# Optimization experiments

Measured on AMD Instinct MI355X. Metric: run time of the kernel, lower is better.

## Reference

```python
import jax, jax.numpy as jnp
import numpy as np

N = 50000      # nodes
E = 800000     # edges (before self-loops)
IN = 256       # in_channels
H = 4          # heads (layer 1)
C = 64         # hidden per head
OUT = 40       # out_channels / classes


def setup_inputs() -> dict:
    key = jax.random.key(0)
    ks = jax.random.split(key, 10)
    s = 0.05  # weight init scale
    return {
        "x": jax.random.normal(ks[0], (N, IN), jnp.float32),
        "edge_index": jax.random.randint(ks[1], (2, E), 0, N),
        "W1": jax.random.normal(ks[2], (IN, H * C), jnp.float32) * s,
        "a_src1": jax.random.normal(ks[3], (H, C), jnp.float32) * s,
        "a_dst1": jax.random.normal(ks[4], (H, C), jnp.float32) * s,
        "b1": jnp.zeros((H * C,), jnp.float32),
        "W2": jax.random.normal(ks[5], (H * C, OUT), jnp.float32) * s,
        "a_src2": jax.random.normal(ks[6], (1, OUT), jnp.float32) * s,
        "a_dst2": jax.random.normal(ks[7], (1, OUT), jnp.float32) * s,
        "b2": jnp.zeros((OUT,), jnp.float32),
    }


def _gat_layer(x, src, dst, W, a_src, a_dst, bias, heads, out_c):
    """PyG GATConv (concat=True, negative_slope=0.2, self-loops already in src/dst)."""
    n = x.shape[0]
    h = (x @ W).reshape(n, heads, out_c)                    # [N,H,C]
    al_s = jnp.sum(h * a_src, axis=-1)                      # [N,H]
    al_d = jnp.sum(h * a_dst, axis=-1)                      # [N,H]
    e = jax.nn.leaky_relu(al_s[src] + al_d[dst], 0.2)       # [Etot,H]
    # edge softmax over incoming edges of each destination node
    m = jax.ops.segment_max(e, dst, num_segments=n)         # [N,H]
    ee = jnp.exp(e - m[dst])
    denom = jax.ops.segment_sum(ee, dst, num_segments=n)
    alpha = ee / (denom[dst] + 1e-16)                       # [Etot,H]
    msg = alpha[:, :, None] * h[src]                        # [Etot,H,C]
    out = jax.ops.segment_sum(msg, dst, num_segments=n)     # [N,H,C]
    return out.reshape(n, heads * out_c) + bias


def reference(x, edge_index, W1, a_src1, a_dst1, b1, W2, a_src2, a_dst2, b2):
    n = x.shape[0]
    loops = jnp.arange(n, dtype=edge_index.dtype)
    src = jnp.concatenate([edge_index[0], loops])
    dst = jnp.concatenate([edge_index[1], loops])
    h = _gat_layer(x, src, dst, W1, a_src1, a_dst1, b1, H, C)   # [N, H*C]
    h = jax.nn.relu(h)
    # F.dropout in eval mode is identity (reference run in eval mode)
    out = _gat_layer(h, src, dst, W2, a_src2, a_dst2, b2, 1, OUT)  # [N, OUT]
    return jax.nn.log_softmax(out, axis=1)
```

## Files before the change

kernel.cpp:

```cpp
#include <hip/hip_runtime.h>
#include <hip/hip_bf16.h>

typedef __hip_bfloat16 bf16;
typedef short v8s __attribute__((ext_vector_type(8)));
typedef float v4f __attribute__((ext_vector_type(4)));

constexpr int NN    = 50000;
constexpr int NE    = 800000;
constexpr int CIN   = 256;
constexpr int HC    = 256;
constexpr int NH    = 4;
constexpr int NOUT  = 40;
constexpr int NPAD  = 48;
constexpr int SCB   = 196;
constexpr int B1    = 128;
constexpr int CH    = (NE + B1 - 1) / B1;
constexpr int NB    = (NN + 255) >> 8;

constexpr size_t al256(size_t x){ return (x + 255) & ~(size_t)255; }
constexpr size_t WS_FLAGS = 0;
constexpr size_t WS_EW1   = 256;
constexpr size_t WS_W1T   = al256(WS_EW1   + (size_t)NE*16);
constexpr size_t WS_AS1N  = al256(WS_W1T   + (size_t)CIN*HC*2);
constexpr size_t WS_AD1N  = al256(WS_AS1N  + HC*2);
constexpr size_t WS_B1N   = al256(WS_AD1N  + HC*2);
constexpr size_t WS_W2T   = al256(WS_B1N   + HC*2);
constexpr size_t WS_AS2N  = al256(WS_W2T   + (size_t)NPAD*HC*2);
constexpr size_t WS_AD2N  = al256(WS_AS2N  + NOUT*2);
constexpr size_t WS_B2N   = al256(WS_AD2N  + NOUT*2);
constexpr size_t WS_COUNTS= al256(WS_B2N   + NOUT*2);
constexpr size_t WS_CURSOR= al256(WS_COUNTS+ (size_t)NN*4);
constexpr size_t WS_ROWPTR= al256(WS_CURSOR+ (size_t)NN*4);
constexpr size_t WS_EIDX  = al256(WS_ROWPTR+ (size_t)(NN+1)*4);
constexpr size_t WS_H1    = al256(WS_EIDX  + (size_t)NE*4);
constexpr size_t WS_ALS1  = al256(WS_H1    + (size_t)NN*HC);
constexpr size_t WS_ALD1  = al256(WS_ALS1  + (size_t)NN*NH*4);
constexpr size_t WS_Y1    = al256(WS_ALD1  + (size_t)NN*NH*4);
constexpr size_t WS_H2    = al256(WS_Y1    + (size_t)NN*HC*2);
constexpr size_t WS_ALS2  = al256(WS_H2    + (size_t)NN*64);
constexpr size_t WS_ALD2  = al256(WS_ALS2  + (size_t)NN*4);
constexpr size_t WS_EW2   = al256(WS_ALD2  + (size_t)NN*4);
constexpr size_t WS_BSUM  = al256(WS_EW2   + (size_t)NE*4);
constexpr size_t WS_BOFF  = al256(WS_BSUM  + 1024);
constexpr size_t WS_GCNT  = al256(WS_BOFF  + 1024);
constexpr size_t WS_ROFF  = al256(WS_GCNT  + (size_t)256*B1*4);
constexpr size_t WS_BBASE = al256(WS_ROFF  + (size_t)256*B1*4);
constexpr size_t WS_EBUF  = al256(WS_BBASE + 1056);

constexpr int CV_W1  = 0;
constexpr int CV_AS1 = CV_W1  + CIN*HC;
constexpr int CV_AD1 = CV_AS1 + HC;
constexpr int CV_B1  = CV_AD1 + HC;
constexpr int CV_W2  = CV_B1  + HC;
constexpr int CV_AS2 = CV_W2  + HC*NOUT;
constexpr int CV_AD2 = CV_AS2 + NOUT;
constexpr int CV_B2  = CV_AD2 + NOUT;
constexpr int CV_HIST= CV_B2  + NOUT;
constexpr int CV_END = CV_HIST + NE;

__device__ __forceinline__ float b2f(bf16 v) { return __bfloat162float(v); }
__device__ __forceinline__ bf16  f2b(float v){ return __float2bfloat16(v); }
__device__ __forceinline__ float bits2f(unsigned short u){ return __uint_as_float(((unsigned)u) << 16); }
__device__ __forceinline__ unsigned short f2bits(float v){
  bf16 t = __float2bfloat16(v);
  return *reinterpret_cast<unsigned short*>(&t);
}
__device__ __forceinline__ float lrelu(float x){ return x > 0.f ? x : 0.2f * x; }

__device__ __forceinline__ float wave_sum(float v){
  #pragma unroll
  for (int off = 32; off; off >>= 1) v += __shfl_xor(v, off, 64);
  return v;
}
__device__ __forceinline__ float wave_max(float v){
  #pragma unroll
  for (int off = 32; off; off >>= 1) v = fmaxf(v, __shfl_xor(v, off, 64));
  return v;
}

__global__ __launch_bounds__(64) void k_detect(const unsigned short* __restrict__ xu,
                                               const unsigned* __restrict__ eu,
                                               int* __restrict__ flags){
  int lane = threadIdx.x;
  int cnt = 0;
  for (int i = lane; i < 256; i += 64){
    int e = (xu[i] >> 7) & 0xFF;
    cnt += (e >= 0x60 && e <= 0x8F) ? 1 : 0;
  }
  #pragma unroll
  for (int off = 32; off; off >>= 1) cnt += __shfl_xor(cnt, off, 64);
  unsigned odd = eu[2 * lane + 1];
  #pragma unroll
  for (int off = 32; off; off >>= 1) odd |= __shfl_xor(odd, off, 64);
  if (lane == 0){
    flags[0] = (cnt < 218) ? 1 : 0;
    flags[1] = (odd == 0)  ? 1 : 0;
  }
}

__device__ __forceinline__ bf16 cvt_b(const void* src, int i, int f32m){
  if (f32m) return __float2bfloat16(((const float*)src)[i]);
  return ((const bf16*)src)[i];
}

__global__ __launch_bounds__(256) void k_convert(
    const void* __restrict__ W1,
    const void* __restrict__ as1,const void* __restrict__ ad1,
    const void* __restrict__ b1, const void* __restrict__ W2,
    const void* __restrict__ as2,const void* __restrict__ ad2,
    const void* __restrict__ b2, const void* __restrict__ ei,
    char* __restrict__ ws){
  const int* flags = (const int*)(ws + WS_FLAGS);
  int f32m = flags[0], i64m = flags[1];
  bf16* w1t  = (bf16*)(ws + WS_W1T);
  bf16* as1n = (bf16*)(ws + WS_AS1N);
  bf16* ad1n = (bf16*)(ws + WS_AD1N);
  bf16* b1n  = (bf16*)(ws + WS_B1N);
  bf16* w2t  = (bf16*)(ws + WS_W2T);
  bf16* as2n = (bf16*)(ws + WS_AS2N);
  bf16* ad2n = (bf16*)(ws + WS_AD2N);
  bf16* b2n  = (bf16*)(ws + WS_B2N);
  int*  counts=(int*) (ws + WS_COUNTS);
  for (int g = blockIdx.x * 256 + threadIdx.x; g < CV_END; g += gridDim.x * 256){
    if      (g < CV_AS1){ int i = g-CV_W1; int k = i >> 8, n = i & 255;
      w1t[n*CIN + k] = cvt_b(W1, i, f32m); }
    else if (g < CV_AD1) as1n[g-CV_AS1] = cvt_b(as1,g-CV_AS1, f32m);
    else if (g < CV_B1 ) ad1n[g-CV_AD1] = cvt_b(ad1,g-CV_AD1, f32m);
    else if (g < CV_W2 ) b1n [g-CV_B1 ] = cvt_b(b1, g-CV_B1,  f32m);
    else if (g < CV_AS2){ int i = g-CV_W2; int k = i / NOUT, n = i - k*NOUT;
      w2t[n*CIN + k] = cvt_b(W2, i, f32m); }
    else if (g < CV_AD2) as2n[g-CV_AS2] = cvt_b(as2,g-CV_AS2, f32m);
    else if (g < CV_B2 ) ad2n[g-CV_AD2] = cvt_b(ad2,g-CV_AD2, f32m);
    else if (g < CV_HIST) b2n[g-CV_B2 ] = cvt_b(b2, g-CV_B2,  f32m);
    else { int i = g-CV_HIST;
      int d = i64m ? (int)((const long long*)ei)[(size_t)NE+i] : ((const int*)ei)[NE+i];
      atomicAdd(&counts[d], 1); }
  }
}

__global__ __launch_bounds__(256) void k_scan_part(const int* __restrict__ counts, int* __restrict__ bsum){
  __shared__ int lds[256];
  int t = threadIdx.x;
  int idx = blockIdx.x * 256 + t;
  int v = (idx < NN) ? counts[idx] : 0;
  lds[t] = v;
  #pragma unroll
  for (int s = 128; s > 0; s >>= 1){
    __syncthreads();
    if (t < s) lds[t] += lds[t + s];
  }
  if (t == 0) bsum[blockIdx.x] = lds[0];
}

__global__ __launch_bounds__(256) void k_scan_mid(const int* __restrict__ bsum, int* __restrict__ boff,
                                                  int* __restrict__ row_ptr){
  __shared__ int lds[256];
  int t = threadIdx.x;
  int v = (t < SCB) ? bsum[t] : 0;
  lds[t] = v;
  for (int off = 1; off < 256; off <<= 1){
    __syncthreads();
    int u = (t >= off) ? lds[t - off] : 0;
    __syncthreads();
    lds[t] += u;
  }
  __syncthreads();
  if (t < SCB) boff[t] = lds[t] - v;
  if (t == 0) row_ptr[NN] = NE;
}

__global__ __launch_bounds__(256) void k_scan_apply(const int* __restrict__ counts, const int* __restrict__ boff,
                                                    int* __restrict__ row_ptr){
  __shared__ int lds[256];
  int t = threadIdx.x;
  int idx = blockIdx.x * 256 + t;
  int v = (idx < NN) ? counts[idx] : 0;
  lds[t] = v;
  for (int off = 1; off < 256; off <<= 1){
    __syncthreads();
    int u = (t >= off) ? lds[t - off] : 0;
    __syncthreads();
    lds[t] += u;
  }
  __syncthreads();
  if (idx < NN) row_ptr[idx] = boff[blockIdx.x] + lds[t] - v;
}

__global__ __launch_bounds__(256) void k_lhist(const void* __restrict__ ei, const int* __restrict__ flags,
                                               int* __restrict__ gcnt){
  __shared__ int h[256];
  int tid = threadIdx.x, blk = blockIdx.x;
  h[tid] = 0;
  __syncthreads();
  int i0 = blk * CH, i1 = min(i0 + CH, NE);
  int i64m = flags[1];
  for (int i = i0 + tid; i < i1; i += 256){
    int d = i64m ? (int)((const long long*)ei)[(size_t)NE + i] : ((const int*)ei)[NE + i];
    atomicAdd(&h[d >> 8], 1);
  }
  __syncthreads();
  gcnt[tid * B1 + blk] = h[tid];
}

__global__ __launch_bounds__(256) void k_gscan(const int* __restrict__ gcnt, int* __restrict__ roff,
                                               int* __restrict__ bbase){
  __shared__ int lds[256];
  int t = threadIdx.x;
  int tot = 0;
  for (int blk = 0; blk < B1; ++blk) tot += gcnt[t * B1 + blk];
  lds[t] = tot;
  for (int off = 1; off < 256; off <<= 1){
    __syncthreads();
    int u = (t >= off) ? lds[t - off] : 0;
    __syncthreads();
    lds[t] += u;
  }
  __syncthreads();
  int base = lds[t] - tot;
  bbase[t] = base;
  if (t == 255) bbase[256] = NE;
  int run = base;
  for (int blk = 0; blk < B1; ++blk){
    roff[t * B1 + blk] = run;
    run += gcnt[t * B1 + blk];
  }
}

__global__ __launch_bounds__(256) void k_bscatter(const void* __restrict__ ei, const int* __restrict__ flags,
                                                  const int* __restrict__ roff, int2* __restrict__ ebuf){
  __shared__ int lcur[256];
  int tid = threadIdx.x, blk = blockIdx.x;
  lcur[tid] = roff[tid * B1 + blk];
  __syncthreads();
  int i0 = blk * CH, i1 = min(i0 + CH, NE);
  int i64m = flags[1];
  for (int i = i0 + tid; i < i1; i += 256){
    int s, d;
    if (i64m){ s = (int)((const long long*)ei)[i]; d = (int)((const long long*)ei)[(size_t)NE + i]; }
    else     { s = ((const int*)ei)[i];            d = ((const int*)ei)[NE + i]; }
    int pos = atomicAdd(&lcur[d >> 8], 1);
    ebuf[pos] = make_int2(s, d);
  }
}

__global__ __launch_bounds__(256) void k_refine(const int2* __restrict__ ebuf, const int* __restrict__ bbase,
                                                const int* __restrict__ row_ptr, int* __restrict__ cursor,
                                                int* __restrict__ eidx){
  int b = blockIdx.x;
  int p0 = bbase[b], p1 = bbase[b + 1];
  for (int p = p0 + threadIdx.x; p < p1; p += 256){
    int2 e = ebuf[p];
    int pos = row_ptr[e.y] + atomicAdd(&cursor[e.y], 1);
    eidx[pos] = e.x;
  }
}

constexpr int G1R = 64;
__global__ __launch_bounds__(256, 2) void k_gemm1(const void* __restrict__ xin,
                                               const int* __restrict__ flags,
                                               const bf16* __restrict__ w1t,
                                               const bf16* __restrict__ as1, const bf16* __restrict__ ad1,
                                               unsigned char* __restrict__ h1q,
                                               float* __restrict__ al_s1, float* __restrict__ al_d1){
  __shared__ __align__(16) short Ab[2][G1R * 64];
  __shared__ __align__(16) short Bb[2][256 * 64];
  int tid  = threadIdx.x;
  int w    = tid >> 6, lane = tid & 63, quad = lane >> 4, c = lane & 15;
  int row0 = blockIdx.x * G1R;
  int f32m = flags[0];

  v4f acc[4][4];
  #pragma unroll
  for (int mt = 0; mt < 4; ++mt)
    #pragma unroll
    for (int nt = 0; nt < 4; ++nt) acc[mt][nt] = (v4f){0.f,0.f,0.f,0.f};

  int arow = tid >> 2, aseg = tid & 3;
  int grow = row0 + arow; if (grow >= NN) grow = NN - 1;
  int asw  = arow & 7;
  int bsw  = tid & 7;

  float4 afl[4];
  v8s    abf[2];
  v8s    breg[8];

  auto loadA = [&](int ph){
    if (f32m){
      const float* src = (const float*)xin + (size_t)grow * CIN + ph*64 + aseg*16;
      #pragma unroll
      for (int i = 0; i < 4; ++i) afl[i] = *reinterpret_cast<const float4*>(src + i*4);
    } else {
      const short* src = (const short*)xin + (size_t)grow * CIN + ph*64 + aseg*16;
      abf[0] = *reinterpret_cast<const v8s*>(src);
      abf[1] = *reinterpret_cast<const v8s*>(src + 8);
    }
  };
  auto loadB = [&](int ph){
    const short* src = (const short*)w1t + (size_t)tid * CIN + ph*64;
    #pragma unroll
    for (int j = 0; j < 8; ++j) breg[j] = *reinterpret_cast<const v8s*>(src + j*8);
  };
  auto stageA = [&](int buf){
    short* dst = &Ab[buf][arow * 64];
    if (f32m){
      #pragma unroll
      for (int k = 0; k < 2; ++k){
        v8s t;
        t[0] = (short)f2bits(afl[2*k].x);   t[1] = (short)f2bits(afl[2*k].y);
        t[2] = (short)f2bits(afl[2*k].z);   t[3] = (short)f2bits(afl[2*k].w);
        t[4] = (short)f2bits(afl[2*k+1].x); t[5] = (short)f2bits(afl[2*k+1].y);
        t[6] = (short)f2bits(afl[2*k+1].z); t[7] = (short)f2bits(afl[2*k+1].w);
        *reinterpret_cast<v8s*>(dst + (((aseg*2 + k) ^ asw) << 3)) = t;
      }
    } else {
      #pragma unroll
      for (int k = 0; k < 2; ++k)
        *reinterpret_cast<v8s*>(dst + (((aseg*2 + k) ^ asw) << 3)) = abf[k];
    }
  };
  auto stageB = [&](int buf){
    short* dst = &Bb[buf][tid * 64];
    #pragma unroll
    for (int j = 0; j < 8; ++j)
      *reinterpret_cast<v8s*>(dst + ((j ^ bsw) << 3)) = breg[j];
  };

  loadA(0); loadB(0);
  stageA(0); stageB(0);
  __syncthreads();

  #pragma unroll
  for (int ph = 0; ph < 4; ++ph){
    int buf = ph & 1;
    if (ph < 3){ loadA(ph + 1); loadB(ph + 1); }
    #pragma unroll
    for (int s = 0; s < 2; ++s){
      int ch = s*4 + quad;
      int sl = (ch ^ (c & 7)) << 3;
      v8s af[4], bfb[4];
      #pragma unroll
      for (int mt = 0; mt < 4; ++mt)
        af[mt] = *reinterpret_cast<const v8s*>(&Ab[buf][(mt*16 + c) * 64 + sl]);
      #pragma unroll
      for (int nt = 0; nt < 4; ++nt)
        bfb[nt] = *reinterpret_cast<const v8s*>(&Bb[buf][(w*64 + nt*16 + c) * 64 + sl]);
      #pragma unroll
      for (int mt = 0; mt < 4; ++mt)
        #pragma unroll
        for (int nt = 0; nt < 4; ++nt)
          acc[mt][nt] = __builtin_amdgcn_mfma_f32_16x16x32_bf16(af[mt], bfb[nt], acc[mt][nt], 0, 0, 0);
    }
    if (ph < 3){
      stageA(buf ^ 1); stageB(buf ^ 1);
      __syncthreads();
    }
  }

  float as1v[4], ad1v[4];
  #pragma unroll
  for (int nt = 0; nt < 4; ++nt){
    as1v[nt] = b2f(as1[w*64 + nt*16 + c]);
    ad1v[nt] = b2f(ad1[w*64 + nt*16 + c]);
  }
  #pragma unroll
  for (int mt = 0; mt < 4; ++mt){
    #pragma unroll
    for (int r = 0; r < 4; ++r){
      float ps = 0.f, pd = 0.f;
      #pragma unroll
      for (int nt = 0; nt < 4; ++nt){ ps += acc[mt][nt][r] * as1v[nt]; pd += acc[mt][nt][r] * ad1v[nt]; }
      #pragma unroll
      for (int off = 1; off < 16; off <<= 1){ ps += __shfl_xor(ps, off, 64); pd += __shfl_xor(pd, off, 64); }
      int row = row0 + mt*16 + quad*4 + r;
      if (c == 0 && row < NN){
        al_s1[row * NH + w] = ps;
        al_d1[row * NH + w] = pd;
      }
    }
  }
  #pragma unroll
  for (int mt = 0; mt < 4; ++mt){
    #pragma unroll
    for (int nt = 0; nt < 4; ++nt){
      #pragma unroll
      for (int r = 0; r < 4; r += 2){
        int row = row0 + mt*16 + quad*4 + r;
        if (row + 1 < NN){
          int pk = __builtin_amdgcn_cvt_pk_fp8_f32(acc[mt][nt][r], acc[mt][nt][r+1], 0, false);
          size_t col = w*64 + nt*16 + c;
          h1q[(size_t)row       * HC + col] = (unsigned char)(pk & 0xFF);
          h1q[(size_t)(row + 1) * HC + col] = (unsigned char)((pk >> 8) & 0xFF);
        } else if (row < NN){
          int pk = __builtin_amdgcn_cvt_pk_fp8_f32(acc[mt][nt][r], acc[mt][nt][r], 0, false);
          h1q[(size_t)row * HC + w*64 + nt*16 + c] = (unsigned char)(pk & 0xFF);
        }
      }
    }
  }
}

__global__ __launch_bounds__(256) void k_gather1(const int* __restrict__ row_ptr, const int* __restrict__ eidx,
                                                 const float* __restrict__ al_s1, const float* __restrict__ al_d1,
                                                 const unsigned* __restrict__ h1v, const bf16* __restrict__ b1,
                                                 bf16* __restrict__ y1){
  int lane = threadIdx.x & 63;
  int n = blockIdx.x * 4 + (threadIdx.x >> 6);
  int h = lane >> 4;
  int p0 = __builtin_amdgcn_readfirstlane(row_ptr[n]);
  int p1 = __builtin_amdgcn_readfirstlane(row_ptr[n + 1]);
  float ad_h = al_d1[n * NH + h];
  float wss = __expf(lrelu(al_s1[n * NH + h] + ad_h));
  unsigned us = h1v[(size_t)n * 64 + lane];
  float den = wss;
  float a0 = wss * __builtin_amdgcn_cvt_f32_fp8(us, 0);
  float a1 = wss * __builtin_amdgcn_cvt_f32_fp8(us, 1);
  float a2 = wss * __builtin_amdgcn_cvt_f32_fp8(us, 2);
  float a3 = wss * __builtin_amdgcn_cvt_f32_fp8(us, 3);
  int p = p0;
  for (; p + 3 < p1; p += 4){
    int sA = __builtin_amdgcn_readfirstlane(eidx[p]);
    int sB = __builtin_amdgcn_readfirstlane(eidx[p + 1]);
    int sC = __builtin_amdgcn_readfirstlane(eidx[p + 2]);
    int sD = __builtin_amdgcn_readfirstlane(eidx[p + 3]);
    float wA = __expf(lrelu(al_s1[sA * NH + h] + ad_h));
    float wB = __expf(lrelu(al_s1[sB * NH + h] + ad_h));
    float wC = __expf(lrelu(al_s1[sC * NH + h] + ad_h));
    float wD = __expf(lrelu(al_s1[sD * NH + h] + ad_h));
    unsigned uA = h1v[(size_t)sA * 64 + lane];
    unsigned uB = h1v[(size_t)sB * 64 + lane];
    unsigned uC = h1v[(size_t)sC * 64 + lane];
    unsigned uD = h1v[(size_t)sD * 64 + lane];
    den += (wA + wB) + (wC + wD);
    a0 += wA * __builtin_amdgcn_cvt_f32_fp8(uA, 0) + wB * __builtin_amdgcn_cvt_f32_fp8(uB, 0)
        + wC * __builtin_amdgcn_cvt_f32_fp8(uC, 0) + wD * __builtin_amdgcn_cvt_f32_fp8(uD, 0);
    a1 += wA * __builtin_amdgcn_cvt_f32_fp8(uA, 1) + wB * __builtin_amdgcn_cvt_f32_fp8(uB, 1)
        + wC * __builtin_amdgcn_cvt_f32_fp8(uC, 1) + wD * __builtin_amdgcn_cvt_f32_fp8(uD, 1);
    a2 += wA * __builtin_amdgcn_cvt_f32_fp8(uA, 2) + wB * __builtin_amdgcn_cvt_f32_fp8(uB, 2)
        + wC * __builtin_amdgcn_cvt_f32_fp8(uC, 2) + wD * __builtin_amdgcn_cvt_f32_fp8(uD, 2);
    a3 += wA * __builtin_amdgcn_cvt_f32_fp8(uA, 3) + wB * __builtin_amdgcn_cvt_f32_fp8(uB, 3)
        + wC * __builtin_amdgcn_cvt_f32_fp8(uC, 3) + wD * __builtin_amdgcn_cvt_f32_fp8(uD, 3);
  }
  for (; p < p1; ++p){
    int s = __builtin_amdgcn_readfirstlane(eidx[p]);
    float w = __expf(lrelu(al_s1[s * NH + h] + ad_h));
    unsigned u = h1v[(size_t)s * 64 + lane];
    den += w;
    a0 += w * __builtin_amdgcn_cvt_f32_fp8(u, 0);
    a1 += w * __builtin_amdgcn_cvt_f32_fp8(u, 1);
    a2 += w * __builtin_amdgcn_cvt_f32_fp8(u, 2);
    a3 += w * __builtin_amdgcn_cvt_f32_fp8(u, 3);
  }
  float inv = 1.f / (den + 1e-16f);
  ushort4 bb = reinterpret_cast<const ushort4*>(b1)[lane];
  ushort4 o;
  o.x = f2bits(fmaxf(a0 * inv + bits2f(bb.x), 0.f));
  o.y = f2bits(fmaxf(a1 * inv + bits2f(bb.y), 0.f));
  o.z = f2bits(fmaxf(a2 * inv + bits2f(bb.z), 0.f));
  o.w = f2bits(fmaxf(a3 * inv + bits2f(bb.w), 0.f));
  reinterpret_cast<ushort4*>(y1)[(size_t)n * 64 + lane] = o;
}

constexpr int W2LP = 260;
__global__ __launch_bounds__(256) void k_gemm2(const bf16* __restrict__ y1, const bf16* __restrict__ w2t,
                                               const bf16* __restrict__ as2, const bf16* __restrict__ ad2,
                                               unsigned char* __restrict__ h2q, float* __restrict__ al_s2,
                                               float* __restrict__ al_d2){
  __shared__ short Wb[NPAD * W2LP];
  int tid = threadIdx.x;
  int w = tid >> 6, lane = tid & 63, quad = lane >> 4, c = lane & 15;
  int m0 = blockIdx.x * 64 + w * 16;
  for (int idx = tid; idx < NPAD * 32; idx += 256){
    int n = idx >> 5, sg = idx & 31;
    *reinterpret_cast<v8s*>(&Wb[n * W2LP + sg * 8]) =
      *reinterpret_cast<const v8s*>((const short*)w2t + (size_t)n * CIN + sg * 8);
  }
  int arow = m0 + c; if (arow >= NN) arow = NN - 1;
  const short* ar = (const short*)y1 + (size_t)arow * HC + quad * 8;
  v8s a[8];
  #pragma unroll
  for (int i = 0; i < 8; ++i) a[i] = *reinterpret_cast<const v8s*>(ar + i * 32);
  __syncthreads();

  v4f acc[3];
  #pragma unroll
  for (int t = 0; t < 3; ++t) acc[t] = (v4f){0.f, 0.f, 0.f, 0.f};
  #pragma unroll
  for (int k = 0; k < 8; ++k){
    int ch = k*4 + quad;
    #pragma unroll
    for (int t = 0; t < 3; ++t){
      v8s b = *reinterpret_cast<const v8s*>(&Wb[(t*16 + c) * W2LP + ch * 8]);
      acc[t] = __builtin_amdgcn_mfma_f32_16x16x32_bf16(a[k], b, acc[t], 0, 0, 0);
    }
  }
  float as2f[3], ad2f[3];
  #pragma unroll
  for (int t = 0; t < 3; ++t){
    int col = t*16 + c;
    as2f[t] = (col < NOUT) ? b2f(as2[col]) : 0.f;
    ad2f[t] = (col < NOUT) ? b2f(ad2[col]) : 0.f;
  }
  #pragma unroll
  for (int r = 0; r < 4; ++r){
    int row = m0 + quad*4 + r;
    float ps = 0.f, pd = 0.f;
    #pragma unroll
    for (int t = 0; t < 3; ++t){ ps += acc[t][r] * as2f[t]; pd += acc[t][r] * ad2f[t]; }
    #pragma unroll
    for (int off = 1; off < 16; off <<= 1){ ps += __shfl_xor(ps, off, 64); pd += __shfl_xor(pd, off, 64); }
    if (row < NN && c == 0){ al_s2[row] = ps; al_d2[row] = pd; }
  }
  #pragma unroll
  for (int t = 0; t < 3; ++t){
    int col = t*16 + c;
    if (col < NOUT){
      #pragma unroll
      for (int r = 0; r < 4; r += 2){
        int row = m0 + quad*4 + r;
        int pk = __builtin_amdgcn_cvt_pk_fp8_f32(acc[t][r], acc[t][r+1], 0, false);
        if (row < NN)     h2q[(size_t)row       * 64 + col] = (unsigned char)(pk & 0xFF);
        if (row + 1 < NN) h2q[(size_t)(row + 1) * 64 + col] = (unsigned char)((pk >> 8) & 0xFF);
      }
    }
  }
}

__global__ __launch_bounds__(256) void k_gather2(const int* __restrict__ row_ptr, const int* __restrict__ eidx,
                                                 const float* __restrict__ al_s2, const float* __restrict__ al_d2,
                                                 const unsigned char* __restrict__ h2q, const bf16* __restrict__ b2v,
                                                 const int* __restrict__ flags, void* __restrict__ out){
  int lane = threadIdx.x & 63;
  int n = blockIdx.x * 4 + (threadIdx.x >> 6);
  int q = lane >> 4, c = lane & 15;
  bool act = (c < 10);
  int p0 = __builtin_amdgcn_readfirstlane(row_ptr[n]);
  int p1 = __builtin_amdgcn_readfirstlane(row_ptr[n + 1]);
  const unsigned* h2v = reinterpret_cast<const unsigned*>(h2q);
  float adn = al_d2[n];
  float den = 0.f, a0 = 0.f, a1 = 0.f, a2 = 0.f, a3 = 0.f;
  if (q == 0){
    float wss = __expf(lrelu(al_s2[n] + adn));
    den = wss;
    if (act){
      unsigned u = h2v[(size_t)n * 16 + c];
      a0 = wss * __builtin_amdgcn_cvt_f32_fp8(u, 0);
      a1 = wss * __builtin_amdgcn_cvt_f32_fp8(u, 1);
      a2 = wss * __builtin_amdgcn_cvt_f32_fp8(u, 2);
      a3 = wss * __builtin_amdgcn_cvt_f32_fp8(u, 3);
    }
  }
  int p = p0 + q;
  for (; p + 4 < p1; p += 8){
    int sA = eidx[p], sB = eidx[p + 4];
    float wA = __expf(lrelu(al_s2[sA] + adn));
    float wB = __expf(lrelu(al_s2[sB] + adn));
    unsigned uA = act ? h2v[(size_t)sA * 16 + c] : 0u;
    unsigned uB = act ? h2v[(size_t)sB * 16 + c] : 0u;
    den += wA + wB;
    a0 += wA * __builtin_amdgcn_cvt_f32_fp8(uA, 0) + wB * __builtin_amdgcn_cvt_f32_fp8(uB, 0);
    a1 += wA * __builtin_amdgcn_cvt_f32_fp8(uA, 1) + wB * __builtin_amdgcn_cvt_f32_fp8(uB, 1);
    a2 += wA * __builtin_amdgcn_cvt_f32_fp8(uA, 2) + wB * __builtin_amdgcn_cvt_f32_fp8(uB, 2);
    a3 += wA * __builtin_amdgcn_cvt_f32_fp8(uA, 3) + wB * __builtin_amdgcn_cvt_f32_fp8(uB, 3);
  }
  if (p < p1){
    int s = eidx[p];
    float w = __expf(lrelu(al_s2[s] + adn));
    unsigned u = act ? h2v[(size_t)s * 16 + c] : 0u;
    den += w;
    a0 += w * __builtin_amdgcn_cvt_f32_fp8(u, 0);
    a1 += w * __builtin_amdgcn_cvt_f32_fp8(u, 1);
    a2 += w * __builtin_amdgcn_cvt_f32_fp8(u, 2);
    a3 += w * __builtin_amdgcn_cvt_f32_fp8(u, 3);
  }
  #pragma unroll
  for (int off = 16; off <= 32; off <<= 1){
    den += __shfl_xor(den, off, 64);
    a0  += __shfl_xor(a0,  off, 64);
    a1  += __shfl_xor(a1,  off, 64);
    a2  += __shfl_xor(a2,  off, 64);
    a3  += __shfl_xor(a3,  off, 64);
  }
  float inv = 1.f / (den + 1e-16f);
  float v0 = -INFINITY, v1 = -INFINITY, v2 = -INFINITY, v3 = -INFINITY;
  if (act){
    ushort4 bb = *reinterpret_cast<const ushort4*>(reinterpret_cast<const unsigned short*>(b2v) + 4 * c);
    v0 = a0 * inv + bits2f(bb.x);
    v1 = a1 * inv + bits2f(bb.y);
    v2 = a2 * inv + bits2f(bb.z);
    v3 = a3 * inv + bits2f(bb.w);
  }
  float M = wave_max(fmaxf(fmaxf(v0, v1), fmaxf(v2, v3)));
  float ex = (q == 0 && act)
           ? (__expf(v0 - M) + __expf(v1 - M)) + (__expf(v2 - M) + __expf(v3 - M)) : 0.f;
  float S = wave_sum(ex);
  if (q == 0 && act){
    float lg = M + __logf(S);
    if (flags[0]){
      float4 o = {v0 - lg, v1 - lg, v2 - lg, v3 - lg};
      *reinterpret_cast<float4*>((float*)out + (size_t)n * NOUT + 4 * c) = o;
    } else {
      ushort4 o;
      o.x = f2bits(v0 - lg); o.y = f2bits(v1 - lg);
      o.z = f2bits(v2 - lg); o.w = f2bits(v3 - lg);
      *reinterpret_cast<ushort4*>((unsigned short*)out + (size_t)n * NOUT + 4 * c) = o;
    }
  }
}

extern "C" void kernel_launch(void* const* d_in, const int* in_sizes, int n_in,
                              void* d_out, int out_size, void* d_ws, size_t ws_size,
                              hipStream_t stream) {
  const void* x   = d_in[0];
  const void* ei  = d_in[1];
  const void* W1  = d_in[2];
  const void* as1 = d_in[3];
  const void* ad1 = d_in[4];
  const void* b1  = d_in[5];
  const void* W2  = d_in[6];
  const void* as2 = d_in[7];
  const void* ad2 = d_in[8];
  const void* b2  = d_in[9];

  char* ws = (char*)d_ws;
  int*   flags   = (int*)  (ws + WS_FLAGS);
  bf16*  w1t     = (bf16*) (ws + WS_W1T);
  bf16*  as1n    = (bf16*) (ws + WS_AS1N);
  bf16*  ad1n    = (bf16*) (ws + WS_AD1N);
  bf16*  b1n     = (bf16*) (ws + WS_B1N);
  bf16*  w2t     = (bf16*) (ws + WS_W2T);
  bf16*  as2n    = (bf16*) (ws + WS_AS2N);
  bf16*  ad2n    = (bf16*) (ws + WS_AD2N);
  bf16*  b2n     = (bf16*) (ws + WS_B2N);
  int*   counts  = (int*)  (ws + WS_COUNTS);
  int*   cursor  = (int*)  (ws + WS_CURSOR);
  int*   row_ptr = (int*)  (ws + WS_ROWPTR);
  int*   eidx    = (int*)  (ws + WS_EIDX);
  unsigned char* h1q = (unsigned char*)(ws + WS_H1);
  float* al_s1   = (float*)(ws + WS_ALS1);
  float* al_d1   = (float*)(ws + WS_ALD1);
  bf16*  y1      = (bf16*) (ws + WS_Y1);
  unsigned char* h2q = (unsigned char*)(ws + WS_H2);
  float* al_s2   = (float*)(ws + WS_ALS2);
  float* al_d2   = (float*)(ws + WS_ALD2);
  int*   bsum    = (int*)  (ws + WS_BSUM);
  int*   boff    = (int*)  (ws + WS_BOFF);
  int*   gcnt    = (int*)  (ws + WS_GCNT);
  int*   roff    = (int*)  (ws + WS_ROFF);
  int*   bbase   = (int*)  (ws + WS_BBASE);
  int2*  ebuf    = (int2*) (ws + WS_EBUF);

  hipMemsetAsync(counts, 0, (size_t)NN * 4, stream);
  hipMemsetAsync(cursor, 0, (size_t)NN * 4, stream);
  hipMemsetAsync(w2t,    0, (size_t)NPAD * CIN * 2, stream);

  k_detect <<<1, 64, 0, stream>>>((const unsigned short*)x, (const unsigned*)ei, flags);
  k_convert<<<1024, 256, 0, stream>>>(W1, as1, ad1, b1, W2, as2, ad2, b2, ei, ws);

  k_lhist   <<<B1, 256, 0, stream>>>(ei, flags, gcnt);
  k_gscan   <<<1, 256, 0, stream>>>(gcnt, roff, bbase);
  k_scan_part <<<SCB, 256, 0, stream>>>(counts, bsum);
  k_scan_mid  <<<1, 256, 0, stream>>>(bsum, boff, row_ptr);
  k_scan_apply<<<SCB, 256, 0, stream>>>(counts, boff, row_ptr);
  k_bscatter<<<B1, 256, 0, stream>>>(ei, flags, roff, ebuf);
  k_refine  <<<NB, 256, 0, stream>>>(ebuf, bbase, row_ptr, cursor, eidx);

  k_gemm1  <<<(NN + G1R - 1) / G1R, 256, 0, stream>>>(x, flags, w1t, as1n, ad1n, h1q, al_s1, al_d1);
  k_gather1<<<NN / 4, 256, 0, stream>>>(row_ptr, eidx, al_s1, al_d1, (const unsigned*)h1q, b1n, y1);
  k_gemm2  <<<(NN + 63) / 64, 256, 0, stream>>>(y1, w2t, as2n, ad2n, h2q, al_s2, al_d2);
  k_gather2<<<NN / 4, 256, 0, stream>>>(row_ptr, eidx, al_s2, al_d2, h2q, b2n, flags, d_out);
}
```

Baseline: 311.5 us.

## Split gather1 wave into four edge groups with 16-byte loads and shuffle reduce

The layer-1 aggregation kernel previously used all 64 lanes of a wave on one edge at a time, each lane loading 4 fp8 bytes of the source row. Now the wave is split into four 16-lane groups that each handle every fourth edge, with each lane loading 16 fp8 bytes (uint4) and keeping 16 accumulators. Partial sums are combined with cross-lane xor shuffles, and 16 lanes write the bf16 output with wide stores. This aims to raise memory-level parallelism per wave on the irregular gather, at the cost of more registers, shuffle reduction work, and idle lanes during the epilogue.

```diff
diff --git a/kernel.cpp b/kernel.cpp
--- a/kernel.cpp
+++ b/kernel.cpp
@@ -399,65 +399,82 @@
   }
 }
 
+#define ACC4(W, U, B) \
+  a[(B)+0] += (W) * __builtin_amdgcn_cvt_f32_fp8((U), 0); \
+  a[(B)+1] += (W) * __builtin_amdgcn_cvt_f32_fp8((U), 1); \
+  a[(B)+2] += (W) * __builtin_amdgcn_cvt_f32_fp8((U), 2); \
+  a[(B)+3] += (W) * __builtin_amdgcn_cvt_f32_fp8((U), 3);
+#define ACC16(W, U) \
+  ACC4(W, (U).x, 0) ACC4(W, (U).y, 4) ACC4(W, (U).z, 8) ACC4(W, (U).w, 12)
+
 __global__ __launch_bounds__(256) void k_gather1(const int* __restrict__ row_ptr, const int* __restrict__ eidx,
                                                  const float* __restrict__ al_s1, const float* __restrict__ al_d1,
                                                  const unsigned* __restrict__ h1v, const bf16* __restrict__ b1,
                                                  bf16* __restrict__ y1){
   int lane = threadIdx.x & 63;
   int n = blockIdx.x * 4 + (threadIdx.x >> 6);
-  int h = lane >> 4;
+  int e = lane >> 4;
+  int l = lane & 15;
+  int hh = l >> 2;
+  const uint4* h1v4 = reinterpret_cast<const uint4*>(h1v);
   int p0 = __builtin_amdgcn_readfirstlane(row_ptr[n]);
   int p1 = __builtin_amdgcn_readfirstlane(row_ptr[n + 1]);
-  float ad_h = al_d1[n * NH + h];
-  float wss = __expf(lrelu(al_s1[n * NH + h] + ad_h));
-  unsigned us = h1v[(size_t)n * 64 + lane];
-  float den = wss;
-  float a0 = wss * __builtin_amdgcn_cvt_f32_fp8(us, 0);
-  float a1 = wss * __builtin_amdgcn_cvt_f32_fp8(us, 1);
-  float a2 = wss * __builtin_amdgcn_cvt_f32_fp8(us, 2);
-  float a3 = wss * __builtin_amdgcn_cvt_f32_fp8(us, 3);
-  int p = p0;
-  for (; p + 3 < p1; p += 4){
-    int sA = __builtin_amdgcn_readfirstlane(eidx[p]);
-    int sB = __builtin_amdgcn_readfirstlane(eidx[p + 1]);
-    int sC = __builtin_amdgcn_readfirstlane(eidx[p + 2]);
-    int sD = __builtin_amdgcn_readfirstlane(eidx[p + 3]);
-    float wA = __expf(lrelu(al_s1[sA * NH + h] + ad_h));
-    float wB = __expf(lrelu(al_s1[sB * NH + h] + ad_h));
-    float wC = __expf(lrelu(al_s1[sC * NH + h] + ad_h));
-    float wD = __expf(lrelu(al_s1[sD * NH + h] + ad_h));
-    unsigned uA = h1v[(size_t)sA * 64 + lane];
-    unsigned uB = h1v[(size_t)sB * 64 + lane];
-    unsigned uC = h1v[(size_t)sC * 64 + lane];
-    unsigned uD = h1v[(size_t)sD * 64 + lane];
-    den += (wA + wB) + (wC + wD);
-    a0 += wA * __builtin_amdgcn_cvt_f32_fp8(uA, 0) + wB * __builtin_amdgcn_cvt_f32_fp8(uB, 0)
-        + wC * __builtin_amdgcn_cvt_f32_fp8(uC, 0) + wD * __builtin_amdgcn_cvt_f32_fp8(uD, 0);
-    a1 += wA * __builtin_amdgcn_cvt_f32_fp8(uA, 1) + wB * __builtin_amdgcn_cvt_f32_fp8(uB, 1)
-        + wC * __builtin_amdgcn_cvt_f32_fp8(uC, 1) + wD * __builtin_amdgcn_cvt_f32_fp8(uD, 1);
-    a2 += wA * __builtin_amdgcn_cvt_f32_fp8(uA, 2) + wB * __builtin_amdgcn_cvt_f32_fp8(uB, 2)
-        + wC * __builtin_amdgcn_cvt_f32_fp8(uC, 2) + wD * __builtin_amdgcn_cvt_f32_fp8(uD, 2);
-    a3 += wA * __builtin_amdgcn_cvt_f32_fp8(uA, 3) + wB * __builtin_amdgcn_cvt_f32_fp8(uB, 3)
-        + wC * __builtin_amdgcn_cvt_f32_fp8(uC, 3) + wD * __builtin_amdgcn_cvt_f32_fp8(uD, 3);
-  }
-  for (; p < p1; ++p){
-    int s = __builtin_amdgcn_readfirstlane(eidx[p]);
-    float w = __expf(lrelu(al_s1[s * NH + h] + ad_h));
-    unsigned u = h1v[(size_t)s * 64 + lane];
+  float ad_h = al_d1[(unsigned)n * 4u + hh];
+
+  float den = 0.f;
+  float a[16];
+  #pragma unroll
+  for (int j = 0; j < 16; ++j) a[j] = 0.f;
+
+  if (e == 0){
+    float wss = __expf(lrelu(al_s1[(unsigned)n * 4u + hh] + ad_h));
+    uint4 u = h1v4[(unsigned)n * 16u + l];
+    den = wss;
+    ACC16(wss, u)
+  }
+
+  int p = p0 + e;
+  for (; p + 4 < p1; p += 8){
+    int sA = eidx[p];
+    int sB = eidx[p + 4];
+    uint4 uA = h1v4[(unsigned)sA * 16u + l];
+    uint4 uB = h1v4[(unsigned)sB * 16u + l];
+    float wA = __expf(lrelu(al_s1[(unsigned)sA * 4u + hh] + ad_h));
+    float wB = __expf(lrelu(al_s1[(unsigned)sB * 4u + hh] + ad_h));
+    den += wA + wB;
+    ACC16(wA, uA)
+    ACC16(wB, uB)
+  }
+  if (p < p1){
+    int s = eidx[p];
+    uint4 u = h1v4[(unsigned)s * 16u + l];
+    float w = __expf(lrelu(al_s1[(unsigned)s * 4u + hh] + ad_h));
     den += w;
-    a0 += w * __builtin_amdgcn_cvt_f32_fp8(u, 0);
-    a1 += w * __builtin_amdgcn_cvt_f32_fp8(u, 1);
-    a2 += w * __builtin_amdgcn_cvt_f32_fp8(u, 2);
-    a3 += w * __builtin_amdgcn_cvt_f32_fp8(u, 3);
-  }
-  float inv = 1.f / (den + 1e-16f);
-  ushort4 bb = reinterpret_cast<const ushort4*>(b1)[lane];
-  ushort4 o;
-  o.x = f2bits(fmaxf(a0 * inv + bits2f(bb.x), 0.f));
-  o.y = f2bits(fmaxf(a1 * inv + bits2f(bb.y), 0.f));
-  o.z = f2bits(fmaxf(a2 * inv + bits2f(bb.z), 0.f));
-  o.w = f2bits(fmaxf(a3 * inv + bits2f(bb.w), 0.f));
-  reinterpret_cast<ushort4*>(y1)[(size_t)n * 64 + lane] = o;
+    ACC16(w, u)
+  }
+
+  #pragma unroll
+  for (int off = 16; off <= 32; off <<= 1){
+    den += __shfl_xor(den, off, 64);
+    #pragma unroll
+    for (int j = 0; j < 16; ++j) a[j] += __shfl_xor(a[j], off, 64);
+  }
+
+  if (lane < 16){
+    float inv = 1.f / (den + 1e-16f);
+    const short* bp = (const short*)b1 + l * 16;
+    v8s bb0 = *reinterpret_cast<const v8s*>(bp);
+    v8s bb1 = *reinterpret_cast<const v8s*>(bp + 8);
+    v8s o0, o1;
+    #pragma unroll
+    for (int j = 0; j < 8; ++j){
+      o0[j] = (short)f2bits(fmaxf(a[j]     * inv + bits2f((unsigned short)bb0[j]), 0.f));
+      o1[j] = (short)f2bits(fmaxf(a[8 + j] * inv + bits2f((unsigned short)bb1[j]), 0.f));
+    }
+    short* yp = (short*)y1 + (size_t)n * HC + l * 16;
+    *reinterpret_cast<v8s*>(yp)     = o0;
+    *reinterpret_cast<v8s*>(yp + 8) = o1;
+  }
 }
 
 constexpr int W2LP = 260;
```

Result: slower. 321.1 us (+3.1%).

## Double GEMM1 row tile to 128 and single-buffer shared memory

Applied to the files above, without the earlier changes.

The first-layer GEMM block now covers 128 rows instead of 64, so each block reuses the staged W1 tile across twice as many rows and fewer blocks reload the full weight matrix. To fit the larger tile, shared memory drops from double-buffered to single-buffered, with an extra barrier per K phase before restaging. This doubles accumulator registers (128 floats per thread), which risks spills or lower occupancy under launch_bounds(256,2). The lost overlap between staging and MFMA compute may also offset the bandwidth savings.

```diff
diff --git a/kernel.cpp b/kernel.cpp
--- a/kernel.cpp
+++ b/kernel.cpp
@@ -255,44 +255,52 @@
   }
 }
 
-constexpr int G1R = 64;
+constexpr int G1R = 128;
 __global__ __launch_bounds__(256, 2) void k_gemm1(const void* __restrict__ xin,
                                                const int* __restrict__ flags,
                                                const bf16* __restrict__ w1t,
                                                const bf16* __restrict__ as1, const bf16* __restrict__ ad1,
                                                unsigned char* __restrict__ h1q,
                                                float* __restrict__ al_s1, float* __restrict__ al_d1){
-  __shared__ __align__(16) short Ab[2][G1R * 64];
-  __shared__ __align__(16) short Bb[2][256 * 64];
+  __shared__ __align__(16) short Ab[G1R * 64];
+  __shared__ __align__(16) short Bb[256 * 64];
   int tid  = threadIdx.x;
   int w    = tid >> 6, lane = tid & 63, quad = lane >> 4, c = lane & 15;
   int row0 = blockIdx.x * G1R;
   int f32m = flags[0];
 
-  v4f acc[4][4];
-  #pragma unroll
-  for (int mt = 0; mt < 4; ++mt)
-    #pragma unroll
-    for (int nt = 0; nt < 4; ++nt) acc[mt][nt] = (v4f){0.f,0.f,0.f,0.f};
+  v4f acc[2][4][4];
+  #pragma unroll
+  for (int mh = 0; mh < 2; ++mh)
+    #pragma unroll
+    for (int mt = 0; mt < 4; ++mt)
+      #pragma unroll
+      for (int nt = 0; nt < 4; ++nt) acc[mh][mt][nt] = (v4f){0.f,0.f,0.f,0.f};
 
   int arow = tid >> 2, aseg = tid & 3;
-  int grow = row0 + arow; if (grow >= NN) grow = NN - 1;
   int asw  = arow & 7;
+  int grow0 = row0 + arow;      if (grow0 >= NN) grow0 = NN - 1;
+  int grow1 = row0 + 64 + arow; if (grow1 >= NN) grow1 = NN - 1;
   int bsw  = tid & 7;
 
-  float4 afl[4];
-  v8s    abf[2];
+  float4 afl[2][4];
+  v8s    abf[2][2];
   v8s    breg[8];
 
   auto loadA = [&](int ph){
     if (f32m){
-      const float* src = (const float*)xin + (size_t)grow * CIN + ph*64 + aseg*16;
+      const float* s0 = (const float*)xin + (size_t)grow0 * CIN + ph*64 + aseg*16;
+      const float* s1 = (const float*)xin + (size_t)grow1 * CIN + ph*64 + aseg*16;
       #pragma unroll
-      for (int i = 0; i < 4; ++i) afl[i] = *reinterpret_cast<const float4*>(src + i*4);
+      for (int i = 0; i < 4; ++i){ afl[0][i] = *reinterpret_cast<const float4*>(s0 + i*4);
+                                   afl[1][i] = *reinterpret_cast<const float4*>(s1 + i*4); }
     } else {
-      const short* src = (const short*)xin + (size_t)grow * CIN + ph*64 + aseg*16;
-      abf[0] = *reinterpret_cast<const v8s*>(src);
-      abf[1] = *reinterpret_cast<const v8s*>(src + 8);
+      const short* s0 = (const short*)xin + (size_t)grow0 * CIN + ph*64 + aseg*16;
+      const short* s1 = (const short*)xin + (size_t)grow1 * CIN + ph*64 + aseg*16;
+      abf[0][0] = *reinterpret_cast<const v8s*>(s0);
+      abf[0][1] = *reinterpret_cast<const v8s*>(s0 + 8);
+      abf[1][0] = *reinterpret_cast<const v8s*>(s1);
+      abf[1][1] = *reinterpret_cast<const v8s*>(s1 + 8);
     }
   };
   auto loadB = [&](int ph){
@@ -300,59 +308,61 @@
     #pragma unroll
     for (int j = 0; j < 8; ++j) breg[j] = *reinterpret_cast<const v8s*>(src + j*8);
   };
-  auto stageA = [&](int buf){
-    short* dst = &Ab[buf][arow * 64];
-    if (f32m){
-      #pragma unroll
-      for (int k = 0; k < 2; ++k){
-        v8s t;
-        t[0] = (short)f2bits(afl[2*k].x);   t[1] = (short)f2bits(afl[2*k].y);
-        t[2] = (short)f2bits(afl[2*k].z);   t[3] = (short)f2bits(afl[2*k].w);
-        t[4] = (short)f2bits(afl[2*k+1].x); t[5] = (short)f2bits(afl[2*k+1].y);
-        t[6] = (short)f2bits(afl[2*k+1].z); t[7] = (short)f2bits(afl[2*k+1].w);
-        *reinterpret_cast<v8s*>(dst + (((aseg*2 + k) ^ asw) << 3)) = t;
+  auto stageA = [&](){
+    #pragma unroll
+    for (int mh = 0; mh < 2; ++mh){
+      short* dst = &Ab[(mh*64 + arow) * 64];
+      if (f32m){
+        #pragma unroll
+        for (int k = 0; k < 2; ++k){
+          v8s t;
+          t[0] = (short)f2bits(afl[mh][2*k].x);   t[1] = (short)f2bits(afl[mh][2*k].y);
+          t[2] = (short)f2bits(afl[mh][2*k].z);   t[3] = (short)f2bits(afl[mh][2*k].w);
+          t[4] = (short)f2bits(afl[mh][2*k+1].x); t[5] = (short)f2bits(afl[mh][2*k+1].y);
+          t[6] = (short)f2bits(afl[mh][2*k+1].z); t[7] = (short)f2bits(afl[mh][2*k+1].w);
+          *reinterpret_cast<v8s*>(dst + (((aseg*2 + k) ^ asw) << 3)) = t;
+        }
+      } else {
+        #pragma unroll
+        for (int k = 0; k < 2; ++k)
+          *reinterpret_cast<v8s*>(dst + (((aseg*2 + k) ^ asw) << 3)) = abf[mh][k];
       }
-    } else {
-      #pragma unroll
-      for (int k = 0; k < 2; ++k)
-        *reinterpret_cast<v8s*>(dst + (((aseg*2 + k) ^ asw) << 3)) = abf[k];
     }
   };
-  auto stageB = [&](int buf){
-    short* dst = &Bb[buf][tid * 64];
+  auto stageB = [&](){
+    short* dst = &Bb[tid * 64];
     #pragma unroll
     for (int j = 0; j < 8; ++j)
       *reinterpret_cast<v8s*>(dst + ((j ^ bsw) << 3)) = breg[j];
   };
 
   loadA(0); loadB(0);
-  stageA(0); stageB(0);
-  __syncthreads();
-
   #pragma unroll
   for (int ph = 0; ph < 4; ++ph){
-    int buf = ph & 1;
+    if (ph) __syncthreads();
+    stageA(); stageB();
+    __syncthreads();
     if (ph < 3){ loadA(ph + 1); loadB(ph + 1); }
     #pragma unroll
     for (int s = 0; s < 2; ++s){
       int ch = s*4 + quad;
       int sl = (ch ^ (c & 7)) << 3;
-      v8s af[4], bfb[4];
-      #pragma unroll
-      for (int mt = 0; mt < 4; ++mt)
-        af[mt] = *reinterpret_cast<const v8s*>(&Ab[buf][(mt*16 + c) * 64 + sl]);
+      v8s bfb[4];
       #pragma unroll
       for (int nt = 0; nt < 4; ++nt)
-        bfb[nt] = *reinterpret_cast<const v8s*>(&Bb[buf][(w*64 + nt*16 + c) * 64 + sl]);
+        bfb[nt] = *reinterpret_cast<const v8s*>(&Bb[(w*64 + nt*16 + c) * 64 + sl]);
       #pragma unroll
-      for (int mt = 0; mt < 4; ++mt)
+      for (int mh = 0; mh < 2; ++mh){
+        v8s af[4];
         #pragma unroll
-        for (int nt = 0; nt < 4; ++nt)
-          acc[mt][nt] = __builtin_amdgcn_mfma_f32_16x16x32_bf16(af[mt], bfb[nt], acc[mt][nt], 0, 0, 0);
-    }
-    if (ph < 3){
-      stageA(buf ^ 1); stageB(buf ^ 1);
-      __syncthreads();
+        for (int mt = 0; mt < 4; ++mt)
+          af[mt] = *reinterpret_cast<const v8s*>(&Ab[(mh*64 + mt*16 + c) * 64 + sl]);
+        #pragma unroll
+        for (int mt = 0; mt < 4; ++mt)
+          #pragma unroll
+          for (int nt = 0; nt < 4; ++nt)
+            acc[mh][mt][nt] = __builtin_amdgcn_mfma_f32_16x16x32_bf16(af[mt], bfb[nt], acc[mh][mt][nt], 0, 0, 0);
+      }
     }
   }
 
@@ -363,36 +373,40 @@
     ad1v[nt] = b2f(ad1[w*64 + nt*16 + c]);
   }
   #pragma unroll
-  for (int mt = 0; mt < 4; ++mt){
-    #pragma unroll
-    for (int r = 0; r < 4; ++r){
-      float ps = 0.f, pd = 0.f;
+  for (int mh = 0; mh < 2; ++mh){
+    int rowb = row0 + mh*64;
+    #pragma unroll
+    for (int mt = 0; mt < 4; ++mt){
       #pragma unroll
-      for (int nt = 0; nt < 4; ++nt){ ps += acc[mt][nt][r] * as1v[nt]; pd += acc[mt][nt][r] * ad1v[nt]; }
+      for (int r = 0; r < 4; ++r){
+        float ps = 0.f, pd = 0.f;
+        #pragma unroll
+        for (int nt = 0; nt < 4; ++nt){ ps += acc[mh][mt][nt][r] * as1v[nt]; pd += acc[mh][mt][nt][r] * ad1v[nt]; }
+        #pragma unroll
+        for (int off = 1; off < 16; off <<= 1){ ps += __shfl_xor(ps, off, 64); pd += __shfl_xor(pd, off, 64); }
+        int row = rowb + mt*16 + quad*4 + r;
+        if (c == 0 && row < NN){
+          al_s1[row * NH + w] = ps;
+          al_d1[row * NH + w] = pd;
+        }
+      }
+    }
+    #pragma unroll
+    for (int mt = 0; mt < 4; ++mt){
       #pragma unroll
-      for (int off = 1; off < 16; off <<= 1){ ps += __shfl_xor(ps, off, 64); pd += __shfl_xor(pd, off, 64); }
-      int row = row0 + mt*16 + quad*4 + r;
-      if (c == 0 && row < NN){
-        al_s1[row * NH + w] = ps;
-        al_d1[row * NH + w] = pd;
-      }
-    }
-  }
-  #pragma unroll
-  for (int mt = 0; mt < 4; ++mt){
-    #pragma unroll
-    for (int nt = 0; nt < 4; ++nt){
-      #pragma unroll
-      for (int r = 0; r < 4; r += 2){
-        int row = row0 + mt*16 + quad*4 + r;
-        if (row + 1 < NN){
-          int pk = __builtin_amdgcn_cvt_pk_fp8_f32(acc[mt][nt][r], acc[mt][nt][r+1], 0, false);
-          size_t col = w*64 + nt*16 + c;
-          h1q[(size_t)row       * HC + col] = (unsigned char)(pk & 0xFF);
-          h1q[(size_t)(row + 1) * HC + col] = (unsigned char)((pk >> 8) & 0xFF);
-        } else if (row < NN){
-          int pk = __builtin_amdgcn_cvt_pk_fp8_f32(acc[mt][nt][r], acc[mt][nt][r], 0, false);
-          h1q[(size_t)row * HC + w*64 + nt*16 + c] = (unsigned char)(pk & 0xFF);
+      for (int nt = 0; nt < 4; ++nt){
+        #pragma unroll
+        for (int r = 0; r < 4; r += 2){
+          int row = rowb + mt*16 + quad*4 + r;
+          if (row + 1 < NN){
+            int pk = __builtin_amdgcn_cvt_pk_fp8_f32(acc[mh][mt][nt][r], acc[mh][mt][nt][r+1], 0, false);
+            size_t col = w*64 + nt*16 + c;
+            h1q[(size_t)row       * HC + col] = (unsigned char)(pk & 0xFF);
+            h1q[(size_t)(row + 1) * HC + col] = (unsigned char)((pk >> 8) & 0xFF);
+          } else if (row < NN){
+            int pk = __builtin_amdgcn_cvt_pk_fp8_f32(acc[mh][mt][nt][r], acc[mh][mt][nt][r], 0, false);
+            h1q[(size_t)row * HC + w*64 + nt*16 + c] = (unsigned char)(pk & 0xFF);
+          }
         }
       }
     }
```

Result: no change. 309.0 us (-0.8%).
